# Kernel tuning notes

Measured on AMD Instinct MI355X. Metric: run time of the kernel, lower is better.

## Reference

```python
import jax, jax.numpy as jnp
import numpy as np

D_MODEL, D_K, D_V, H = 1024, 64, 64, 16
B, NQ, NK = 4, 2048, 2048


def setup_inputs() -> dict:
    key = jax.random.key(0)
    ks = jax.random.split(key, 14)
    def xavier(k, fan_in, fan_out):
        lim = np.sqrt(6.0 / (fan_in + fan_out))
        return jax.random.uniform(k, (fan_in, fan_out), jnp.float32, -lim, lim)
    return {
        "queries": jax.random.normal(ks[0], (B, NQ, D_MODEL), jnp.float32),
        "keys": jax.random.normal(ks[1], (B, NK, D_MODEL), jnp.float32),
        "values": jax.random.normal(ks[2], (B, NK, D_MODEL), jnp.float32),
        "language_feature": jax.random.normal(ks[3], (B, NQ, D_MODEL), jnp.float32),
        "Wq": xavier(ks[4], D_MODEL, H * D_K), "bq": jnp.zeros((H * D_K,), jnp.float32),
        "Wk": xavier(ks[5], D_MODEL, H * D_K), "bk": jnp.zeros((H * D_K,), jnp.float32),
        "Wv": xavier(ks[6], D_MODEL, H * D_V), "bv": jnp.zeros((H * D_V,), jnp.float32),
        "Ws": xavier(ks[7], D_MODEL, H * D_K), "bs": jnp.zeros((H * D_K,), jnp.float32),
        "Wo": xavier(ks[8], H * D_V, D_MODEL), "bo": jnp.zeros((D_MODEL,), jnp.float32),
    }


def reference(queries, keys, values, language_feature, Wq, bq, Wk, bk, Wv, bv, Ws, bs, Wo, bo):
    b, nq = queries.shape[:2]
    nk = keys.shape[1]
    scale = 1.0 / np.sqrt(D_K)
    # projections -> [b, h, n, d]
    q = (queries @ Wq + bq).reshape(b, nq, H, D_K).transpose(0, 2, 1, 3)
    s = (language_feature @ Ws + bs).reshape(b, nq, H, D_K).transpose(0, 2, 1, 3)
    k = (keys @ Wk + bk).reshape(b, nk, H, D_K).transpose(0, 2, 1, 3)
    v = (values @ Wv + bv).reshape(b, nk, H, D_V).transpose(0, 2, 1, 3)
    # raw scaled scores [b, h, nq, nk]
    att = jnp.einsum("bhqd,bhkd->bhqk", q, k) * scale
    # language branch: per-query dot(q_i, s_i) -> [b, h, nq]
    lang = jnp.einsum("bhqd,bhqd->bhq", q, s) * scale
    # concatenated softmax over [nk + 1]; only last column (beta) is used
    combined = jax.nn.softmax(jnp.concatenate([att, lang[..., None]], axis=-1), axis=-1)
    beta = combined[..., -1:]  # [b, h, nq, 1]
    # NOTE: original uses RAW (non-softmaxed) att for the value aggregation
    att_v = jnp.einsum("bhqk,bhkd->bhqd", att, v)
    out = beta * s + (1.0 - beta) * att_v  # [b, h, nq, d]
    out = out.transpose(0, 2, 1, 3).reshape(b, nq, H * D_V)
    return out @ Wo + bo
```

## Files before the change

kernel.cpp:

```cpp
#include <hip/hip_runtime.h>


#define SCALE 0.125f
#define LOG2E 1.44269504088896f
#define SCLOG 0.18033688011112042f

typedef __attribute__((ext_vector_type(8))) short bf16x8;
typedef __attribute__((ext_vector_type(4))) short s16x4;
typedef __attribute__((ext_vector_type(4))) float f32x4;
typedef __attribute__((ext_vector_type(16))) float f32x16;

__device__ __forceinline__ float b2f(short x) {
  return __uint_as_float(((unsigned)(unsigned short)x) << 16);
}
__device__ __forceinline__ short f2b(float x) {
  unsigned u = __float_as_uint(x);
  unsigned r = (u + 0x7fffu + ((u >> 16) & 1u)) >> 16;
  return (short)r;
}
__device__ __forceinline__ float fexp2(float x) {
  float r;
  asm("v_exp_f32 %0, %1" : "=v"(r) : "v"(x));
  return r;
}
__device__ __forceinline__ bf16x8 cvt8(f32x4 lo, f32x4 hi) {
  unsigned u0, u1, u2, u3;
  asm("v_cvt_pk_bf16_f32 %0, %1, %2" : "=v"(u0) : "v"(lo[0]), "v"(lo[1]));
  asm("v_cvt_pk_bf16_f32 %0, %1, %2" : "=v"(u1) : "v"(lo[2]), "v"(lo[3]));
  asm("v_cvt_pk_bf16_f32 %0, %1, %2" : "=v"(u2) : "v"(hi[0]), "v"(hi[1]));
  asm("v_cvt_pk_bf16_f32 %0, %1, %2" : "=v"(u3) : "v"(hi[2]), "v"(hi[3]));
  union { unsigned u[4]; bf16x8 v; } r;
  r.u[0] = u0; r.u[1] = u1; r.u[2] = u2; r.u[3] = u3;
  return r.v;
}

__device__ __forceinline__ void gl2lds16(const short* g, short* l) {
  __builtin_amdgcn_global_load_lds(
      (const __attribute__((address_space(1))) unsigned int*)g,
      (__attribute__((address_space(3))) unsigned int*)l, 16, 0, 0);
}

__global__ __launch_bounds__(256) void wtrans_kernel(
    const float* W0, const float* W1, const float* W2, const float* W3, const float* W4,
    short* O0, short* O1, short* O2, short* O3, short* O4) {
  const float* Wp[5] = {W0, W1, W2, W3, W4};
  short* Op[5] = {O0, O1, O2, O3, O4};
  const float* W = Wp[blockIdx.z];
  short* O = Op[blockIdx.z];
  int n0 = blockIdx.x * 64, k0 = blockIdx.y * 64;
  __shared__ float ts[64 * 68];
  int tid = threadIdx.x;
  int r = tid >> 4, c = (tid & 15) * 4;
  for (int ir = 0; ir < 4; ++ir) {
    f32x4 v = *reinterpret_cast<const f32x4*>(&W[(size_t)(k0 + r + ir * 16) * 1024 + n0 + c]);
    *reinterpret_cast<f32x4*>(&ts[(r + ir * 16) * 68 + c]) = v;
  }
  __syncthreads();
  for (int ir = 0; ir < 4; ++ir) {
    int n = r + ir * 16;
    s16x4 o;
    for (int j = 0; j < 4; ++j) o[j] = f2b(ts[(c + j) * 68 + n]);
    *reinterpret_cast<s16x4*>(&O[(size_t)(n0 + n) * 1024 + k0 + c]) = o;
  }
}


#define A_LOAD(T, R0, R1, R2, R3)                                           \
  {                                                                         \
    int kst = (T) * 32;                                                     \
    int row0 = tid >> 2, cc0 = tid & 3;                                     \
    int gc0 = (cc0 ^ ((row0 >> 1) & 3)) * 8;                                \
    const float* ap0 = &Ag[(size_t)(m0 + row0) * 1024 + kst + gc0];         \
    R0 = *reinterpret_cast<const f32x4*>(ap0);                              \
    R1 = *reinterpret_cast<const f32x4*>(ap0 + 4);                          \
    int row1 = row0 + 128;                                                  \
    int gc1 = (cc0 ^ ((row1 >> 1) & 3)) * 8;                                \
    const float* ap1 = &Ag[(size_t)(m0 + row1) * 1024 + kst + gc1];         \
    R2 = *reinterpret_cast<const f32x4*>(ap1);                              \
    R3 = *reinterpret_cast<const f32x4*>(ap1 + 4);                          \
  }

#define A_WRITE(T, R0, R1, R2, R3)                                          \
  {                                                                         \
    short* Ad = &As[(T) & 1][0];                                            \
    *reinterpret_cast<bf16x8*>(&Ad[tid * 8]) = cvt8(R0, R1);                \
    *reinterpret_cast<bf16x8*>(&Ad[(tid + 512) * 8]) = cvt8(R2, R3);        \
  }

#define B_STAGE(T)                                                          \
  {                                                                         \
    int kst = (T) * 32;                                                     \
    short* Bd = &Bs[(T) & 1][0];                                            \
    _Pragma("unroll") for (int it = 0; it < 2; ++it) {                      \
      int s = tid + it * 512;                                               \
      int row = s >> 2, cc = s & 3;                                         \
      int gc = (cc ^ ((row >> 1) & 3)) * 8;                                 \
      gl2lds16(&Bg[(size_t)(n0 + row) * 1024 + kst + gc], &Bd[s * 8]);      \
    }                                                                       \
  }

#define FRAG(BUF, ROW, KC)                                                  \
  (*reinterpret_cast<const bf16x8*>(                                        \
      &(BUF)[(ROW) * 32 + (((KC) ^ (((ROW) >> 1) & 3)) * 8)]))

#define BODY(T, DO_B, DO_A, VM, DO_WRITE, W0, W1, W2, W3, L0, L1, L2, L3)   \
  {                                                                         \
    const short* Ab = &As[(T) & 1][0];                                      \
    const short* Bb = &Bs[(T) & 1][0];                                      \
    bf16x8 a[2][2], b[2][2];                                                \
    _Pragma("unroll") for (int mi = 0; mi < 2; ++mi)                        \
      _Pragma("unroll") for (int kk = 0; kk < 2; ++kk)                      \
        a[mi][kk] = FRAG(Ab, wr + mi * 32 + l31, kk * 2 + l5);              \
    _Pragma("unroll") for (int ni = 0; ni < 2; ++ni)                        \
      _Pragma("unroll") for (int kk = 0; kk < 2; ++kk)                      \
        b[ni][kk] = FRAG(Bb, wc + ni * 32 + l31, kk * 2 + l5);              \
    if (DO_B) B_STAGE((T) + 1);                                             \
    __builtin_amdgcn_s_setprio(1);                                          \
    _Pragma("unroll") for (int kk = 0; kk < 2; ++kk)                        \
      _Pragma("unroll") for (int ni = 0; ni < 2; ++ni)                      \
        _Pragma("unroll") for (int mi = 0; mi < 2; ++mi)                    \
          acc32[mi][ni] = __builtin_amdgcn_mfma_f32_32x32x16_bf16(          \
              a[mi][kk], b[ni][kk], acc32[mi][ni], 0, 0, 0);                \
    __builtin_amdgcn_s_setprio(0);                                          \
    __builtin_amdgcn_s_barrier();                                           \
    bf16x8 a2[2][2];                                                        \
    _Pragma("unroll") for (int mi = 0; mi < 2; ++mi)                        \
      _Pragma("unroll") for (int kk = 0; kk < 2; ++kk)                      \
        a2[mi][kk] = FRAG(Ab, wr + 64 + mi * 32 + l31, kk * 2 + l5);        \
    if (DO_A) A_LOAD((T) + 3, L0, L1, L2, L3);                              \
    asm volatile("s_waitcnt vmcnt(" #VM ")" ::: "memory");                  \
    if (DO_WRITE) A_WRITE((T) + 1, W0, W1, W2, W3);                         \
    __builtin_amdgcn_s_setprio(1);                                          \
    _Pragma("unroll") for (int kk = 0; kk < 2; ++kk)                        \
      _Pragma("unroll") for (int ni = 0; ni < 2; ++ni)                      \
        _Pragma("unroll") for (int mi = 0; mi < 2; ++mi)                    \
          acc32[mi + 2][ni] = __builtin_amdgcn_mfma_f32_32x32x16_bf16(      \
              a2[mi][kk], b[ni][kk], acc32[mi + 2][ni], 0, 0, 0);           \
    __builtin_amdgcn_s_setprio(0);                                          \
    asm volatile("s_waitcnt lgkmcnt(0)" ::: "memory");                      \
    __builtin_amdgcn_s_barrier();                                           \
  }

#define GEMM_CORE()                                                         \
  f32x4 p0, p1, p2, p3, q0, q1, q2, q3, r0, r1, r2, r3;                     \
  B_STAGE(0); A_LOAD(0, p0, p1, p2, p3);                                    \
  A_LOAD(1, q0, q1, q2, q3);                                                \
  A_LOAD(2, r0, r1, r2, r3);                                                \
  asm volatile("s_waitcnt vmcnt(8)" ::: "memory");                          \
  A_WRITE(0, p0, p1, p2, p3);                                               \
  asm volatile("s_waitcnt lgkmcnt(0)" ::: "memory");                        \
  __builtin_amdgcn_s_barrier();                                             \
  for (int t = 0; t < 27; t += 3) {                                         \
    BODY(t, true, true, 4, true, q0, q1, q2, q3, p0, p1, p2, p3);           \
    BODY(t + 1, true, true, 4, true, r0, r1, r2, r3, q0, q1, q2, q3);       \
    BODY(t + 2, true, true, 4, true, p0, p1, p2, p3, r0, r1, r2, r3);       \
  }                                                                         \
  BODY(27, true, true, 4, true, q0, q1, q2, q3, p0, p1, p2, p3);            \
  BODY(28, true, true, 4, true, r0, r1, r2, r3, q0, q1, q2, q3);            \
  BODY(29, true, false, 0, true, p0, p1, p2, p3, p0, p1, p2, p3);           \
  BODY(30, true, false, 0, true, q0, q1, q2, q3, p0, p1, p2, p3);           \
  BODY(31, false, false, 0, false, p0, p1, p2, p3, p0, p1, p2, p3);

__global__ __launch_bounds__(512, 2) void proj_gemm_kernel(
    const float* A0, const float* A1, const float* A2, const float* A3,
    const short* W0, const short* W1, const short* W2, const short* W3,
    const float* c0, const float* c1, const float* c2, const float* c3,
    short* O0, short* O1, short* O2, short* O3) {
  const float* Ap[4] = {A0, A1, A2, A3};
  const short* Wp[4] = {W0, W1, W2, W3};
  const float* bp[4] = {c0, c1, c2, c3};
  short* Op[4] = {O0, O1, O2, O3};

  int id = blockIdx.x;
  int work = (id & 7) * 64 + (id >> 3);
  int z = work >> 7;
  int rem = work & 127;
  int my = rem >> 2;
  int nx = rem & 3;
  const float* Ag = Ap[z];
  const short* Bg = Wp[z];
  const float* bias = bp[z];
  short* Out = Op[z];
  int m0 = my * 256, n0 = nx * 256;

  __shared__ short As[2][8192];
  __shared__ short Bs[2][8192];
  int tid = threadIdx.x;
  int wave = tid >> 6, lane = tid & 63;
  int l31 = lane & 31, l5 = lane >> 5;
  int wr = (wave >> 2) * 128, wc = (wave & 3) * 64;

  f32x16 acc32[4][2] = {};

  GEMM_CORE();

#pragma unroll
  for (int ni = 0; ni < 2; ++ni) {
    int n = n0 + wc + ni * 32 + l31;
    float bi = bias[n];
    int hh = n >> 6, d = n & 63;
#pragma unroll
    for (int mi = 0; mi < 4; ++mi)
#pragma unroll
      for (int reg = 0; reg < 16; ++reg) {
        int m = m0 + wr + mi * 32 + (reg & 3) + 8 * (reg >> 2) + 4 * l5;
        int bb = m >> 11, t = m & 2047;
        Out[(size_t)(((bb << 4) + hh) * 2048 + t) * 64 + d] = f2b(acc32[mi][ni][reg] + bi);
      }
  }
}

__global__ __launch_bounds__(256) void final_gemm_kernel(const short* A, const short* Wt,
                                                         const float* bias, float* Out) {
  int id = blockIdx.x;
  int work = (id & 7) * 64 + (id >> 3);
  int my = work >> 3, nx = work & 7;
  int m0 = my * 128, n0 = nx * 128;

  __shared__ short Asl[128 * 64];
  __shared__ short Bsl[128 * 64];
  int tid = threadIdx.x;
  int wave = tid >> 6, lane = tid & 63, lg = lane >> 4, lr = lane & 15;
  int wr = (wave >> 1) * 64, wc = (wave & 1) * 64;
  f32x4 acc[4][4] = {};
  int srow = lane >> 3, scol = (lane & 7) * 8;

  for (int k0 = 0; k0 < 1024; k0 += 64) {
    __syncthreads();
#pragma unroll
    for (int i = 0; i < 4; ++i) {
      int c = i * 4 + wave;
      gl2lds16(&A[(size_t)(m0 + c * 8 + srow) * 1024 + k0 + scol], &Asl[c * 512 + lane * 8]);
      gl2lds16(&Wt[(size_t)(n0 + c * 8 + srow) * 1024 + k0 + scol], &Bsl[c * 512 + lane * 8]);
    }
    __syncthreads();
#pragma unroll
    for (int kk = 0; kk < 2; ++kk) {
      bf16x8 a[4], b[4];
      for (int i = 0; i < 4; ++i)
        a[i] = *reinterpret_cast<const bf16x8*>(&Asl[(wr + i * 16 + lr) * 64 + kk * 32 + lg * 8]);
      for (int j = 0; j < 4; ++j)
        b[j] = *reinterpret_cast<const bf16x8*>(&Bsl[(wc + j * 16 + lr) * 64 + kk * 32 + lg * 8]);
      for (int i = 0; i < 4; ++i)
        for (int j = 0; j < 4; ++j)
          acc[i][j] = __builtin_amdgcn_mfma_f32_16x16x32_bf16(a[i], b[j], acc[i][j], 0, 0, 0);
    }
  }
  for (int j = 0; j < 4; ++j) {
    int n = n0 + wc + j * 16 + lr;
    float bi = bias[n];
    for (int i = 0; i < 4; ++i)
      for (int rr = 0; rr < 4; ++rr) {
        int m = m0 + wr + i * 16 + lg * 4 + rr;
        Out[(size_t)m * 1024 + n] = acc[i][j][rr] + bi;
      }
  }
}

__global__ __launch_bounds__(256) void kv_kernel(const short* Kp, const short* Vp, float* KVp) {
  int c = blockIdx.x, bh = blockIdx.y;
  int tid = threadIdx.x;
  __shared__ float Ks[32 * 64];
  __shared__ float Vs[32 * 64];
  int srow = tid >> 3, scol = (tid & 7) * 8;
  int dk = tid >> 2, dv0 = (tid & 3) * 16;
  float acc[16] = {};
  for (int sub = 0; sub < 8; ++sub) {
    int tkb = c * 256 + sub * 32;
    __syncthreads();
    bf16x8 kv = *reinterpret_cast<const bf16x8*>(&Kp[(size_t)(bh * 2048 + tkb + srow) * 64 + scol]);
    bf16x8 vv = *reinterpret_cast<const bf16x8*>(&Vp[(size_t)(bh * 2048 + tkb + srow) * 64 + scol]);
    f32x4 ka, kb, va, vb;
#pragma unroll
    for (int j = 0; j < 4; ++j) {
      ka[j] = b2f(kv[j]); kb[j] = b2f(kv[j + 4]);
      va[j] = b2f(vv[j]); vb[j] = b2f(vv[j + 4]);
    }
    *reinterpret_cast<f32x4*>(&Ks[srow * 64 + scol]) = ka;
    *reinterpret_cast<f32x4*>(&Ks[srow * 64 + scol + 4]) = kb;
    *reinterpret_cast<f32x4*>(&Vs[srow * 64 + scol]) = va;
    *reinterpret_cast<f32x4*>(&Vs[srow * 64 + scol + 4]) = vb;
    __syncthreads();
    for (int tok = 0; tok < 32; ++tok) {
      float kval = Ks[tok * 64 + dk];
      f32x4 v0 = *reinterpret_cast<const f32x4*>(&Vs[tok * 64 + dv0]);
      f32x4 v1 = *reinterpret_cast<const f32x4*>(&Vs[tok * 64 + dv0 + 4]);
      f32x4 v2 = *reinterpret_cast<const f32x4*>(&Vs[tok * 64 + dv0 + 8]);
      f32x4 v3 = *reinterpret_cast<const f32x4*>(&Vs[tok * 64 + dv0 + 12]);
#pragma unroll
      for (int j = 0; j < 4; ++j) {
        acc[j] += kval * v0[j];
        acc[4 + j] += kval * v1[j];
        acc[8 + j] += kval * v2[j];
        acc[12 + j] += kval * v3[j];
      }
    }
  }
  float* o = &KVp[(size_t)(bh * 8 + c) * 4096 + dk * 64 + dv0];
  for (int j = 0; j < 16; ++j) o[j] = acc[j];
}

__global__ __launch_bounds__(256) void kvred_kernel(const float* KVp, short* KVt) {
  int bh = blockIdx.x;
  for (int e = threadIdx.x; e < 4096; e += 256) {
    float s = 0.f;
    for (int cc = 0; cc < 8; ++cc) s += KVp[(size_t)(bh * 8 + cc) * 4096 + e];
    int dk = e >> 6, dv = e & 63;
    KVt[(size_t)bh * 4096 + dv * 64 + dk] = f2b(s);
  }
}

__global__ __launch_bounds__(256) void beta_combine_kernel(
    const short* Qp, const short* Kp, const short* Sp, const short* KVt, short* X) {
  int bh = blockIdx.y, q0 = blockIdx.x * 64;
  int b = bh >> 4, h = bh & 15;
  int tid = threadIdx.x;
  __shared__ float lsm[64];
  __shared__ float red[4][64];
  __shared__ float betaL[64];
  __shared__ short Ks[2][128 * 64];

  const short* Kb = Kp + (size_t)bh * 2048 * 64;
  int srow = tid >> 3, schunk = tid & 7;
  int sxor = (schunk ^ (srow & 7)) * 8;

#pragma unroll
  for (int cc = 0; cc < 4; ++cc)
    gl2lds16(&Kb[(size_t)(cc * 32 + srow) * 64 + sxor], &Ks[0][cc * 2048 + tid * 8]);

  {
    int row = tid >> 2, seg = tid & 3;
    const short* qr = Qp + (size_t)(bh * 2048 + q0 + row) * 64 + seg * 16;
    const short* sr = Sp + (size_t)(bh * 2048 + q0 + row) * 64 + seg * 16;
    float sum = 0.f;
    for (int cc = 0; cc < 2; ++cc) {
      bf16x8 qv = reinterpret_cast<const bf16x8*>(qr)[cc];
      bf16x8 sv = reinterpret_cast<const bf16x8*>(sr)[cc];
      for (int j = 0; j < 8; ++j) sum += b2f(qv[j]) * b2f(sv[j]);
    }
    sum += __shfl_xor(sum, 1);
    sum += __shfl_xor(sum, 2);
    if (seg == 0) lsm[row] = sum * SCLOG;
  }
  __syncthreads();

  int wave = tid >> 6, lane = tid & 63, lg = lane >> 4, lr = lane & 15;
  const bf16x8* qbase = reinterpret_cast<const bf16x8*>(
      Qp + (size_t)(bh * 2048 + q0 + wave * 16 + lr) * 64);
  bf16x8 a0 = qbase[lg];
  bf16x8 a1 = qbase[4 + lg];
  bf16x8 as0[4], as1[4];
#pragma unroll
  for (int qt = 0; qt < 4; ++qt) {
    const bf16x8* qb = reinterpret_cast<const bf16x8*>(
        Qp + (size_t)(bh * 2048 + q0 + qt * 16 + lr) * 64);
    bf16x8 t0 = qb[lg], t1 = qb[4 + lg];
#pragma unroll
    for (int j = 0; j < 8; ++j) {
      as0[qt][j] = f2b(b2f(t0[j]) * SCLOG);
      as1[qt][j] = f2b(b2f(t1[j]) * SCLOG);
    }
  }

  float s[4][4] = {};
  for (int t = 0; t < 16; ++t) {
    __builtin_amdgcn_s_barrier();
    if (t < 15) {
      const short* src = Kb + (size_t)(t + 1) * 8192;
      short* dst = &Ks[(t + 1) & 1][0];
#pragma unroll
      for (int cc = 0; cc < 4; ++cc)
        gl2lds16(&src[(size_t)(cc * 32 + srow) * 64 + sxor], &dst[cc * 2048 + tid * 8]);
      asm volatile("s_waitcnt vmcnt(4)" ::: "memory");
    } else {
      asm volatile("s_waitcnt vmcnt(0)" ::: "memory");
    }
    __builtin_amdgcn_s_barrier();
    __builtin_amdgcn_sched_barrier(0);
    const short* Kbuf = &Ks[t & 1][0];
    f32x4 sc[4][2];
    __builtin_amdgcn_s_setprio(1);
#pragma unroll
    for (int kt = 0; kt < 2; ++kt) {
      int row = wave * 32 + kt * 16 + lr;
      int xs = row & 7;
      bf16x8 b0 = *reinterpret_cast<const bf16x8*>(&Kbuf[row * 64 + ((lg ^ xs) * 8)]);
      bf16x8 b1 = *reinterpret_cast<const bf16x8*>(&Kbuf[row * 64 + (((4 + lg) ^ xs) * 8)]);
#pragma unroll
      for (int qt = 0; qt < 4; ++qt) {
        f32x4 z = {0.f, 0.f, 0.f, 0.f};
        z = __builtin_amdgcn_mfma_f32_16x16x32_bf16(as0[qt], b0, z, 0, 0, 0);
        z = __builtin_amdgcn_mfma_f32_16x16x32_bf16(as1[qt], b1, z, 0, 0, 0);
        sc[qt][kt] = z;
      }
    }
    __builtin_amdgcn_s_setprio(0);
#pragma unroll
    for (int qt = 0; qt < 4; ++qt)
#pragma unroll
      for (int kt = 0; kt < 2; ++kt) {
        s[qt][0] += fexp2(sc[qt][kt][0]);
        s[qt][1] += fexp2(sc[qt][kt][1]);
        s[qt][2] += fexp2(sc[qt][kt][2]);
        s[qt][3] += fexp2(sc[qt][kt][3]);
      }
  }
#pragma unroll
  for (int qt = 0; qt < 4; ++qt)
#pragma unroll
    for (int rr = 0; rr < 4; ++rr)
      for (int m = 1; m < 16; m <<= 1) s[qt][rr] += __shfl_xor(s[qt][rr], m);
  if (lr == 0) {
#pragma unroll
    for (int qt = 0; qt < 4; ++qt)
#pragma unroll
      for (int rr = 0; rr < 4; ++rr)
        red[wave][qt * 16 + lg * 4 + rr] = s[qt][rr];
  }
  __syncthreads();
  if (tid < 64) {
    float tot = red[0][tid] + red[1][tid] + red[2][tid] + red[3][tid];
    float el = fexp2(lsm[tid]);
    betaL[tid] = el / (tot + el);
  }
  __syncthreads();
  float bt[4];
#pragma unroll
  for (int rr = 0; rr < 4; ++rr) bt[rr] = betaL[wave * 16 + lg * 4 + rr];

  const short* kvb = KVt + (size_t)bh * 4096;
#pragma unroll
  for (int nt = 0; nt < 4; ++nt) {
    const bf16x8* bb8 = reinterpret_cast<const bf16x8*>(&kvb[(nt * 16 + lr) * 64]);
    bf16x8 b0 = bb8[lg], b1 = bb8[4 + lg];
    f32x4 z = {0.f, 0.f, 0.f, 0.f};
    z = __builtin_amdgcn_mfma_f32_16x16x32_bf16(a0, b0, z, 0, 0, 0);
    z = __builtin_amdgcn_mfma_f32_16x16x32_bf16(a1, b1, z, 0, 0, 0);
#pragma unroll
    for (int rr = 0; rr < 4; ++rr) {
      int rl = wave * 16 + lg * 4 + rr;
      int q = q0 + rl;
      float sv = b2f(Sp[(size_t)(bh * 2048 + q) * 64 + nt * 16 + lr]);
      float val = bt[rr] * sv + (1.0f - bt[rr]) * (SCALE * z[rr]);
      X[(size_t)(b * 2048 + q) * 1024 + h * 64 + nt * 16 + lr] = f2b(val);
    }
  }
}

extern "C" void kernel_launch(void* const* d_in, const int* in_sizes, int n_in,
                              void* d_out, int out_size, void* d_ws, size_t ws_size,
                              hipStream_t stream) {
  const float* queries = (const float*)d_in[0];
  const float* keys = (const float*)d_in[1];
  const float* values = (const float*)d_in[2];
  const float* langf = (const float*)d_in[3];
  const float* Wq = (const float*)d_in[4];
  const float* bq = (const float*)d_in[5];
  const float* Wk = (const float*)d_in[6];
  const float* bk = (const float*)d_in[7];
  const float* Wv = (const float*)d_in[8];
  const float* bv = (const float*)d_in[9];
  const float* Ws = (const float*)d_in[10];
  const float* bs = (const float*)d_in[11];
  const float* Wo = (const float*)d_in[12];
  const float* bo = (const float*)d_in[13];
  float* out = (float*)d_out;

  char* ws = (char*)d_ws;
  const size_t MB = 1ull << 20;
  short* Wqt = (short*)(ws + 0 * MB);
  short* Wkt = (short*)(ws + 2 * MB);
  short* Wvt = (short*)(ws + 4 * MB);
  short* Wst = (short*)(ws + 6 * MB);
  short* Wot = (short*)(ws + 8 * MB);
  short* Qp = (short*)(ws + 10 * MB);
  short* Kp = (short*)(ws + 26 * MB);
  short* Vp = (short*)(ws + 42 * MB);
  short* Sp = (short*)(ws + 58 * MB);
  short* X = (short*)(ws + 74 * MB);
  float* KVp = (float*)(ws + 90 * MB);
  short* KVt = (short*)(ws + 98 * MB);

  wtrans_kernel<<<dim3(16, 16, 5), 256, 0, stream>>>(Wq, Wk, Wv, Ws, Wo, Wqt, Wkt, Wvt, Wst, Wot);
  proj_gemm_kernel<<<512, 512, 0, stream>>>(queries, keys, values, langf,
                                            Wqt, Wkt, Wvt, Wst, bq, bk, bv, bs,
                                            Qp, Kp, Vp, Sp);
  kv_kernel<<<dim3(8, 64), 256, 0, stream>>>(Kp, Vp, KVp);
  kvred_kernel<<<64, 256, 0, stream>>>(KVp, KVt);
  beta_combine_kernel<<<dim3(32, 64), 256, 0, stream>>>(Qp, Kp, Sp, KVt, X);
  final_gemm_kernel<<<512, 256, 0, stream>>>(X, Wot, bo, out);
}
```

Before: 228.8 us.

## Run projection GEMM with 1024 threads, each wave owning a 64x64 tile

The projection GEMM block grows from 512 to 1024 threads (16 waves). Each wave now computes a 64x64 output sub-tile instead of 128x64, so accumulator registers halve and the per-wave A and B staging loads halve. The two-phase MFMA body with its mid-iteration barrier becomes a single phase, and the A prefetch and LDS write move ahead of the MFMAs. Risks are lower per-wave MFMA density, more barrier participants, and losing the second resident block per CU that the old launch bounds allowed.

```diff
diff --git a/kernel.cpp b/kernel.cpp
--- a/kernel.cpp
+++ b/kernel.cpp
@@ -65,7 +65,7 @@
 }
 
 
-#define A_LOAD(T, R0, R1, R2, R3)                                           \
+#define A_LOAD(T, R0, R1)                                                   \
   {                                                                         \
     int kst = (T) * 32;                                                     \
     int row0 = tid >> 2, cc0 = tid & 3;                                     \
@@ -73,37 +73,28 @@
     const float* ap0 = &Ag[(size_t)(m0 + row0) * 1024 + kst + gc0];         \
     R0 = *reinterpret_cast<const f32x4*>(ap0);                              \
     R1 = *reinterpret_cast<const f32x4*>(ap0 + 4);                          \
-    int row1 = row0 + 128;                                                  \
-    int gc1 = (cc0 ^ ((row1 >> 1) & 3)) * 8;                                \
-    const float* ap1 = &Ag[(size_t)(m0 + row1) * 1024 + kst + gc1];         \
-    R2 = *reinterpret_cast<const f32x4*>(ap1);                              \
-    R3 = *reinterpret_cast<const f32x4*>(ap1 + 4);                          \
-  }
-
-#define A_WRITE(T, R0, R1, R2, R3)                                          \
+  }
+
+#define A_WRITE(T, R0, R1)                                                  \
   {                                                                         \
     short* Ad = &As[(T) & 1][0];                                            \
     *reinterpret_cast<bf16x8*>(&Ad[tid * 8]) = cvt8(R0, R1);                \
-    *reinterpret_cast<bf16x8*>(&Ad[(tid + 512) * 8]) = cvt8(R2, R3);        \
   }
 
 #define B_STAGE(T)                                                          \
   {                                                                         \
     int kst = (T) * 32;                                                     \
     short* Bd = &Bs[(T) & 1][0];                                            \
-    _Pragma("unroll") for (int it = 0; it < 2; ++it) {                      \
-      int s = tid + it * 512;                                               \
-      int row = s >> 2, cc = s & 3;                                         \
-      int gc = (cc ^ ((row >> 1) & 3)) * 8;                                 \
-      gl2lds16(&Bg[(size_t)(n0 + row) * 1024 + kst + gc], &Bd[s * 8]);      \
-    }                                                                       \
+    int row = tid >> 2, cc = tid & 3;                                       \
+    int gc = (cc ^ ((row >> 1) & 3)) * 8;                                   \
+    gl2lds16(&Bg[(size_t)(n0 + row) * 1024 + kst + gc], &Bd[tid * 8]);      \
   }
 
 #define FRAG(BUF, ROW, KC)                                                  \
   (*reinterpret_cast<const bf16x8*>(                                        \
       &(BUF)[(ROW) * 32 + (((KC) ^ (((ROW) >> 1) & 3)) * 8)]))
 
-#define BODY(T, DO_B, DO_A, VM, DO_WRITE, W0, W1, W2, W3, L0, L1, L2, L3)   \
+#define BODY(T, DO_B, DO_A, VM, DO_WRITE, W0, W1, L0, L1)                   \
   {                                                                         \
     const short* Ab = &As[(T) & 1][0];                                      \
     const short* Bb = &Bs[(T) & 1][0];                                      \
@@ -115,6 +106,9 @@
       _Pragma("unroll") for (int kk = 0; kk < 2; ++kk)                      \
         b[ni][kk] = FRAG(Bb, wc + ni * 32 + l31, kk * 2 + l5);              \
     if (DO_B) B_STAGE((T) + 1);                                             \
+    if (DO_A) A_LOAD((T) + 3, L0, L1);                                      \
+    asm volatile("s_waitcnt vmcnt(" #VM ")" ::: "memory");                  \
+    if (DO_WRITE) A_WRITE((T) + 1, W0, W1);                                 \
     __builtin_amdgcn_s_setprio(1);                                          \
     _Pragma("unroll") for (int kk = 0; kk < 2; ++kk)                        \
       _Pragma("unroll") for (int ni = 0; ni < 2; ++ni)                      \
@@ -122,46 +116,31 @@
           acc32[mi][ni] = __builtin_amdgcn_mfma_f32_32x32x16_bf16(          \
               a[mi][kk], b[ni][kk], acc32[mi][ni], 0, 0, 0);                \
     __builtin_amdgcn_s_setprio(0);                                          \
-    __builtin_amdgcn_s_barrier();                                           \
-    bf16x8 a2[2][2];                                                        \
-    _Pragma("unroll") for (int mi = 0; mi < 2; ++mi)                        \
-      _Pragma("unroll") for (int kk = 0; kk < 2; ++kk)                      \
-        a2[mi][kk] = FRAG(Ab, wr + 64 + mi * 32 + l31, kk * 2 + l5);        \
-    if (DO_A) A_LOAD((T) + 3, L0, L1, L2, L3);                              \
-    asm volatile("s_waitcnt vmcnt(" #VM ")" ::: "memory");                  \
-    if (DO_WRITE) A_WRITE((T) + 1, W0, W1, W2, W3);                         \
-    __builtin_amdgcn_s_setprio(1);                                          \
-    _Pragma("unroll") for (int kk = 0; kk < 2; ++kk)                        \
-      _Pragma("unroll") for (int ni = 0; ni < 2; ++ni)                      \
-        _Pragma("unroll") for (int mi = 0; mi < 2; ++mi)                    \
-          acc32[mi + 2][ni] = __builtin_amdgcn_mfma_f32_32x32x16_bf16(      \
-              a2[mi][kk], b[ni][kk], acc32[mi + 2][ni], 0, 0, 0);           \
-    __builtin_amdgcn_s_setprio(0);                                          \
     asm volatile("s_waitcnt lgkmcnt(0)" ::: "memory");                      \
     __builtin_amdgcn_s_barrier();                                           \
   }
 
 #define GEMM_CORE()                                                         \
-  f32x4 p0, p1, p2, p3, q0, q1, q2, q3, r0, r1, r2, r3;                     \
-  B_STAGE(0); A_LOAD(0, p0, p1, p2, p3);                                    \
-  A_LOAD(1, q0, q1, q2, q3);                                                \
-  A_LOAD(2, r0, r1, r2, r3);                                                \
-  asm volatile("s_waitcnt vmcnt(8)" ::: "memory");                          \
-  A_WRITE(0, p0, p1, p2, p3);                                               \
+  f32x4 p0, p1, q0, q1, r0, r1;                                             \
+  B_STAGE(0); A_LOAD(0, p0, p1);                                            \
+  A_LOAD(1, q0, q1);                                                        \
+  A_LOAD(2, r0, r1);                                                        \
+  asm volatile("s_waitcnt vmcnt(4)" ::: "memory");                          \
+  A_WRITE(0, p0, p1);                                                       \
   asm volatile("s_waitcnt lgkmcnt(0)" ::: "memory");                        \
   __builtin_amdgcn_s_barrier();                                             \
   for (int t = 0; t < 27; t += 3) {                                         \
-    BODY(t, true, true, 4, true, q0, q1, q2, q3, p0, p1, p2, p3);           \
-    BODY(t + 1, true, true, 4, true, r0, r1, r2, r3, q0, q1, q2, q3);       \
-    BODY(t + 2, true, true, 4, true, p0, p1, p2, p3, r0, r1, r2, r3);       \
+    BODY(t, true, true, 2, true, q0, q1, p0, p1);                           \
+    BODY(t + 1, true, true, 2, true, r0, r1, q0, q1);                       \
+    BODY(t + 2, true, true, 2, true, p0, p1, r0, r1);                       \
   }                                                                         \
-  BODY(27, true, true, 4, true, q0, q1, q2, q3, p0, p1, p2, p3);            \
-  BODY(28, true, true, 4, true, r0, r1, r2, r3, q0, q1, q2, q3);            \
-  BODY(29, true, false, 0, true, p0, p1, p2, p3, p0, p1, p2, p3);           \
-  BODY(30, true, false, 0, true, q0, q1, q2, q3, p0, p1, p2, p3);           \
-  BODY(31, false, false, 0, false, p0, p1, p2, p3, p0, p1, p2, p3);
-
-__global__ __launch_bounds__(512, 2) void proj_gemm_kernel(
+  BODY(27, true, true, 2, true, q0, q1, p0, p1);                            \
+  BODY(28, true, true, 2, true, r0, r1, q0, q1);                            \
+  BODY(29, true, false, 0, true, p0, p1, p0, p1);                           \
+  BODY(30, true, false, 0, true, q0, q1, p0, p1);                           \
+  BODY(31, false, false, 0, false, p0, p1, p0, p1);
+
+__global__ __launch_bounds__(1024) void proj_gemm_kernel(
     const float* A0, const float* A1, const float* A2, const float* A3,
     const short* W0, const short* W1, const short* W2, const short* W3,
     const float* c0, const float* c1, const float* c2, const float* c3,
@@ -188,9 +167,9 @@
   int tid = threadIdx.x;
   int wave = tid >> 6, lane = tid & 63;
   int l31 = lane & 31, l5 = lane >> 5;
-  int wr = (wave >> 2) * 128, wc = (wave & 3) * 64;
-
-  f32x16 acc32[4][2] = {};
+  int wr = (wave >> 2) * 64, wc = (wave & 3) * 64;
+
+  f32x16 acc32[2][2] = {};
 
   GEMM_CORE();
 
@@ -200,7 +179,7 @@
     float bi = bias[n];
     int hh = n >> 6, d = n & 63;
 #pragma unroll
-    for (int mi = 0; mi < 4; ++mi)
+    for (int mi = 0; mi < 2; ++mi)
 #pragma unroll
       for (int reg = 0; reg < 16; ++reg) {
         int m = m0 + wr + mi * 32 + (reg & 3) + 8 * (reg >> 2) + 4 * l5;
@@ -482,9 +461,9 @@
   short* KVt = (short*)(ws + 98 * MB);
 
   wtrans_kernel<<<dim3(16, 16, 5), 256, 0, stream>>>(Wq, Wk, Wv, Ws, Wo, Wqt, Wkt, Wvt, Wst, Wot);
-  proj_gemm_kernel<<<512, 512, 0, stream>>>(queries, keys, values, langf,
-                                            Wqt, Wkt, Wvt, Wst, bq, bk, bv, bs,
-                                            Qp, Kp, Vp, Sp);
+  proj_gemm_kernel<<<512, 1024, 0, stream>>>(queries, keys, values, langf,
+                                             Wqt, Wkt, Wvt, Wst, bq, bk, bv, bs,
+                                             Qp, Kp, Vp, Sp);
   kv_kernel<<<dim3(8, 64), 256, 0, stream>>>(Kp, Vp, KVp);
   kvred_kernel<<<64, 256, 0, stream>>>(KVp, KVt);
   beta_combine_kernel<<<dim3(32, 64), 256, 0, stream>>>(Qp, Kp, Sp, KVt, X);
```

Result: slower. 413.5 us (+80.7%).
